# Kernel optimization log

Hardware: AMD Instinct MI355X
Metric: run time of the kernel (lower is better)

Reference implementation:

```python
import jax, jax.numpy as jnp
import numpy as np

NUM_NODES = 100000
D = 256            # node_hidden_dim
H = 256            # edge_hidden_dim
P = 524288         # num_pairs


def setup_inputs() -> dict:
    key = jax.random.key(0)
    k1, k2, k3, k4, k5, k6 = jax.random.split(key, 6)
    h_nodes = jax.random.normal(k1, (NUM_NODES, D), dtype=jnp.float32)
    dst = jax.random.randint(k2, (P,), 0, NUM_NODES, dtype=jnp.int64)
    src = jax.random.randint(k3, (P,), 0, NUM_NODES, dtype=jnp.int64)
    # Bias-free MLP weights, stored as [in, out] so forward is x @ W
    s1 = 1.0 / np.sqrt(2 * D)
    s2 = 1.0 / np.sqrt(H)
    W1 = jax.random.uniform(k4, (2 * D, H), jnp.float32, -s1, s1)
    W2 = jax.random.uniform(k5, (H, H), jnp.float32, -s2, s2)
    W3 = jax.random.uniform(k6, (H, 2), jnp.float32, -s2, s2)
    return {"h_nodes": h_nodes, "dst": dst, "src": src, "W1": W1, "W2": W2, "W3": W3}


def reference(h_nodes, dst, src, W1, W2, W3):
    # gather src/dst embeddings and concat -> [P, 2D]
    h_pair = jnp.concatenate([h_nodes[dst], h_nodes[src]], axis=-1)
    x = jax.nn.relu(h_pair @ W1)   # [P, H]
    x = jax.nn.relu(x @ W2)        # [P, H]
    return x @ W3                  # [P, 2] edge logits
```

## Files before the change

kernel.cpp:

```cpp
#include <hip/hip_runtime.h>
#include <stdint.h>

typedef __attribute__((ext_vector_type(8))) short short8;
typedef __attribute__((ext_vector_type(4))) short short4v;
typedef __attribute__((ext_vector_type(4))) float floatx4;

__device__ __forceinline__ unsigned short f2bf(float x) {
  unsigned int u = __float_as_uint(x);
  u += 0x7fffu + ((u >> 16) & 1u);
  return (unsigned short)(u >> 16);
}
__device__ __forceinline__ float bf2f(unsigned short b) {
  return __uint_as_float(((unsigned int)b) << 16);
}
__device__ __forceinline__ int sw3(int r) { return (r & 7) ^ (((r >> 3) & 1) * 3); }

__global__ void prep_kernel(const float* __restrict__ h, const float* __restrict__ W1,
                            const float* __restrict__ W2, const float* __restrict__ W3,
                            unsigned short* __restrict__ HBF, unsigned short* __restrict__ W1F,
                            unsigned short* __restrict__ W2F, unsigned short* __restrict__ W3F,
                            int nh4) {
  const int t = threadIdx.x;
  int b = blockIdx.x;
  if (b < 512) {
    int u = b * 256 + t;
    int j = u & 7, kq = (u >> 3) & 3, n = (u >> 5) & 255, k32 = u >> 13;
    W1F[u] = f2bf(W1[(k32 * 32 + kq * 8 + j) * 256 + n]);
    return;
  }
  b -= 512;
  if (b < 256) {
    int u = b * 256 + t;
    int j = u & 7, kq = (u >> 3) & 3, n = (u >> 5) & 255, k32 = u >> 13;
    W2F[u] = f2bf(W2[(k32 * 32 + kq * 8 + j) * 256 + n]);
    return;
  }
  b -= 256;
  if (b < 16) {
    int u = b * 256 + t;
    int j = u & 7, L = (u >> 3) & 63, k32 = u >> 9;
    int n = L & 15, kq = L >> 4;
    W3F[u] = (n < 2) ? f2bf(W3[(k32 * 32 + kq * 8 + j) * 2 + n]) : (unsigned short)0;
    return;
  }
  b -= 16;
  int u = b * 256 + t;
  if (u < nh4) {
    float4 v = ((const float4*)h)[u];
    short4v s;
    s[0] = (short)f2bf(v.x); s[1] = (short)f2bf(v.y);
    s[2] = (short)f2bf(v.z); s[3] = (short)f2bf(v.w);
    ((short4v*)HBF)[u] = s;
  }
}

__global__ __launch_bounds__(256, 2)
void edge_mlp3(const unsigned short* __restrict__ hbf,
               const int* __restrict__ dst,
               const int* __restrict__ src,
               const unsigned short* __restrict__ W1F,
               const unsigned short* __restrict__ W2F,
               const unsigned short* __restrict__ W3F,
               float* __restrict__ out) {
  __shared__ unsigned short A[64 * 512];
  __shared__ int ioff[128];
  unsigned short* X  = A;
  unsigned short* X2 = A + 16384;

  const int t = threadIdx.x, lane = t & 63, w = t >> 6;
  const int lq = lane >> 4, lm = lane & 15;
  const int m0 = blockIdx.x * 64;

  if (t < 64)       ioff[t] = dst[m0 + t];
  else if (t < 128) ioff[t] = src[m0 + t - 64];
  __syncthreads();

  {
    const int c = lane, half = (c >= 32) ? 64 : 0, cc = c & 31;
    short8 g[16];
#pragma unroll
    for (int it = 0; it < 16; ++it) {
      int node = ioff[half + it * 4 + w];
      g[it] = ((const short8*)hbf)[node * 32 + cc];
    }
#pragma unroll
    for (int it = 0; it < 16; ++it) {
      int r = it * 4 + w;
      *(short8*)&A[r * 512 + ((c ^ sw3(r)) << 3)] = g[it];
    }
  }

  floatx4 acc[4][4];
#pragma unroll
  for (int i = 0; i < 4; ++i)
#pragma unroll
    for (int j = 0; j < 4; ++j) acc[i][j] = (floatx4)(0.0f);
  __syncthreads();

  const short8* B1 = (const short8*)W1F;
  const short8* B2 = (const short8*)W2F;

  {
    short8 bq[4][4];
#pragma unroll
    for (int s = 0; s < 4; ++s)
#pragma unroll
      for (int jt = 0; jt < 4; ++jt)
        bq[s][jt] = B1[(s * 256 + w * 64 + jt * 16 + lm) * 4 + lq];

#pragma unroll
    for (int s = 0; s < 16; ++s) {
#pragma unroll
      for (int i = 0; i < 4; ++i) {
        int r = i * 16 + lm, cch = s * 4 + lq;
        short8 af = *(const short8*)&A[r * 512 + ((cch ^ sw3(r)) << 3)];
#pragma unroll
        for (int j = 0; j < 4; ++j)
          acc[i][j] = __builtin_amdgcn_mfma_f32_16x16x32_bf16(af, bq[s & 3][j], acc[i][j], 0, 0, 0);
      }
      if (s < 12)
#pragma unroll
        for (int jt = 0; jt < 4; ++jt)
          bq[s & 3][jt] = B1[((s + 4) * 256 + w * 64 + jt * 16 + lm) * 4 + lq];
    }
  }
  __syncthreads();
#pragma unroll
  for (int i = 0; i < 4; ++i) {
    int row0 = i * 16 + lq * 4;
#pragma unroll
    for (int j = 0; j < 4; ++j) {
      int col = w * 64 + j * 16 + lm, c8 = col >> 3, ce = col & 7;
#pragma unroll
      for (int rg = 0; rg < 4; ++rg) {
        int row = row0 + rg;
        float v = acc[i][j][rg];
        v = v > 0.0f ? v : 0.0f;
        X[row * 256 + (((c8 ^ sw3(row)) << 3) | ce)] = f2bf(v);
      }
    }
  }
#pragma unroll
  for (int i = 0; i < 4; ++i)
#pragma unroll
    for (int j = 0; j < 4; ++j) acc[i][j] = (floatx4)(0.0f);
  __syncthreads();

  {
    short8 bq[4][4];
#pragma unroll
    for (int s = 0; s < 4; ++s)
#pragma unroll
      for (int jt = 0; jt < 4; ++jt)
        bq[s][jt] = B2[(s * 256 + w * 64 + jt * 16 + lm) * 4 + lq];

#pragma unroll
    for (int s = 0; s < 8; ++s) {
#pragma unroll
      for (int i = 0; i < 4; ++i) {
        int r = i * 16 + lm, cch = s * 4 + lq;
        short8 af = *(const short8*)&X[r * 256 + ((cch ^ sw3(r)) << 3)];
#pragma unroll
        for (int j = 0; j < 4; ++j)
          acc[i][j] = __builtin_amdgcn_mfma_f32_16x16x32_bf16(af, bq[s & 3][j], acc[i][j], 0, 0, 0);
      }
      if (s < 4)
#pragma unroll
        for (int jt = 0; jt < 4; ++jt)
          bq[s & 3][jt] = B2[((s + 4) * 256 + w * 64 + jt * 16 + lm) * 4 + lq];
    }
  }
  __syncthreads();
#pragma unroll
  for (int i = 0; i < 4; ++i) {
    int row0 = i * 16 + lq * 4;
#pragma unroll
    for (int j = 0; j < 4; ++j) {
      int col = w * 64 + j * 16 + lm, c8 = col >> 3, ce = col & 7;
#pragma unroll
      for (int rg = 0; rg < 4; ++rg) {
        int row = row0 + rg;
        float v = acc[i][j][rg];
        v = v > 0.0f ? v : 0.0f;
        X2[row * 256 + (((c8 ^ sw3(row)) << 3) | ce)] = f2bf(v);
      }
    }
  }
  __syncthreads();

  {
    floatx4 a3 = (floatx4)(0.0f);
    const short8* B3 = (const short8*)W3F;
#pragma unroll
    for (int s = 0; s < 8; ++s) {
      short8 b3 = B3[s * 64 + lane];
      int r = w * 16 + lm, cch = s * 4 + lq;
      short8 af = *(const short8*)&X2[r * 256 + ((cch ^ sw3(r)) << 3)];
      a3 = __builtin_amdgcn_mfma_f32_16x16x32_bf16(af, b3, a3, 0, 0, 0);
    }
    if (lm < 2) {
#pragma unroll
      for (int rg = 0; rg < 4; ++rg)
        out[(m0 + w * 16 + lq * 4 + rg) * 2 + lm] = a3[rg];
    }
  }
}

__global__ void wfrag_kernel(const float* __restrict__ W,
                             unsigned short* __restrict__ out, int total) {
  int u = blockIdx.x * 256 + threadIdx.x;
  if (u >= total) return;
  int j = u & 7, kq = (u >> 3) & 3, n = (u >> 5) & 255, k32 = u >> 13;
  out[u] = f2bf(W[(k32 * 32 + kq * 8 + j) * 256 + n]);
}

__global__ __launch_bounds__(256, 2)
void edge_mlp_fb(const float* __restrict__ h,
                 const int* __restrict__ dst,
                 const int* __restrict__ src,
                 const unsigned short* __restrict__ W1F,
                 const unsigned short* __restrict__ W2F,
                 const float* __restrict__ W3,
                 float* __restrict__ out) {
  __shared__ unsigned short A[64 * 512];
  __shared__ float w3s[512];
  __shared__ int ioff[128];
  unsigned short* X = A;
  const int t = threadIdx.x, lane = t & 63, w = t >> 6;
  const int lq = lane >> 4, lm = lane & 15;
  const int m0 = blockIdx.x * 64;
  if (t < 64) ioff[t] = dst[m0 + t];
  else if (t < 128) ioff[t] = src[m0 + t - 64];
  w3s[t] = W3[t];
  w3s[t + 256] = W3[t + 256];
  __syncthreads();
  {
    const int c = lane, half = (c >= 32) ? 64 : 0, cc = c & 31;
#pragma unroll
    for (int it = 0; it < 16; ++it) {
      int r = it * 4 + w;
      int node = ioff[half + r];
      const float4* h4 = (const float4*)h;
      float4 v0 = h4[node * 64 + cc * 2], v1 = h4[node * 64 + cc * 2 + 1];
      short8 v;
      v[0] = (short)f2bf(v0.x); v[1] = (short)f2bf(v0.y);
      v[2] = (short)f2bf(v0.z); v[3] = (short)f2bf(v0.w);
      v[4] = (short)f2bf(v1.x); v[5] = (short)f2bf(v1.y);
      v[6] = (short)f2bf(v1.z); v[7] = (short)f2bf(v1.w);
      *(short8*)&A[r * 512 + ((c ^ (r & 7)) << 3)] = v;
    }
  }
  floatx4 acc[4][4];
#pragma unroll
  for (int i = 0; i < 4; ++i)
#pragma unroll
    for (int j = 0; j < 4; ++j) acc[i][j] = (floatx4)(0.0f);
  __syncthreads();
  const short8* B1 = (const short8*)W1F;
  const short8* B2 = (const short8*)W2F;
#pragma unroll
  for (int k32 = 0; k32 < 16; ++k32) {
    short8 b[4], af[4];
#pragma unroll
    for (int jt = 0; jt < 4; ++jt)
      b[jt] = B1[(k32 * 256 + w * 64 + jt * 16 + lm) * 4 + lq];
#pragma unroll
    for (int i = 0; i < 4; ++i) {
      int r = i * 16 + lm, c = k32 * 4 + lq;
      af[i] = *(const short8*)&A[r * 512 + ((c ^ (r & 7)) << 3)];
    }
#pragma unroll
    for (int i = 0; i < 4; ++i)
#pragma unroll
      for (int j = 0; j < 4; ++j)
        acc[i][j] = __builtin_amdgcn_mfma_f32_16x16x32_bf16(af[i], b[j], acc[i][j], 0, 0, 0);
  }
  __syncthreads();
#pragma unroll
  for (int i = 0; i < 4; ++i) {
    int row0 = i * 16 + lq * 4;
#pragma unroll
    for (int j = 0; j < 4; ++j) {
      int col = w * 64 + j * 16 + lm, c8 = col >> 3, ce = col & 7;
#pragma unroll
      for (int rg = 0; rg < 4; ++rg) {
        int row = row0 + rg;
        float v = acc[i][j][rg];
        v = v > 0.0f ? v : 0.0f;
        X[row * 256 + (((c8 ^ (row & 7)) << 3) | ce)] = f2bf(v);
      }
    }
  }
#pragma unroll
  for (int i = 0; i < 4; ++i)
#pragma unroll
    for (int j = 0; j < 4; ++j) acc[i][j] = (floatx4)(0.0f);
  __syncthreads();
#pragma unroll
  for (int k32 = 0; k32 < 8; ++k32) {
    short8 b[4], af[4];
#pragma unroll
    for (int jt = 0; jt < 4; ++jt)
      b[jt] = B2[(k32 * 256 + w * 64 + jt * 16 + lm) * 4 + lq];
#pragma unroll
    for (int i = 0; i < 4; ++i) {
      int r = i * 16 + lm, c = k32 * 4 + lq;
      af[i] = *(const short8*)&X[r * 256 + ((c ^ (r & 7)) << 3)];
    }
#pragma unroll
    for (int i = 0; i < 4; ++i)
#pragma unroll
      for (int j = 0; j < 4; ++j)
        acc[i][j] = __builtin_amdgcn_mfma_f32_16x16x32_bf16(af[i], b[j], acc[i][j], 0, 0, 0);
  }
  __syncthreads();
#pragma unroll
  for (int i = 0; i < 4; ++i) {
    int row0 = i * 16 + lq * 4;
#pragma unroll
    for (int j = 0; j < 4; ++j) {
      int col = w * 64 + j * 16 + lm, c8 = col >> 3, ce = col & 7;
#pragma unroll
      for (int rg = 0; rg < 4; ++rg) {
        int row = row0 + rg;
        float v = acc[i][j][rg];
        v = v > 0.0f ? v : 0.0f;
        X[row * 256 + (((c8 ^ (row & 7)) << 3) | ce)] = f2bf(v);
      }
    }
  }
  __syncthreads();
  {
    int r = t >> 2, o = (t >> 1) & 1, hh = t & 1;
    float s = 0.0f;
#pragma unroll
    for (int it = 0; it < 16; ++it) {
      int c = hh * 16 + it;
      short8 xv = *(const short8*)&X[r * 256 + ((c ^ (r & 7)) << 3)];
#pragma unroll
      for (int e = 0; e < 8; ++e)
        s += bf2f((unsigned short)xv[e]) * w3s[((c << 3) + e) * 2 + o];
    }
    s += __shfl_xor(s, 1);
    if (hh == 0) out[(m0 + r) * 2 + o] = s;
  }
}

extern "C" void kernel_launch(void* const* d_in, const int* in_sizes, int n_in,
                              void* d_out, int out_size, void* d_ws, size_t ws_size,
                              hipStream_t stream) {
  const float* h   = (const float*)d_in[0];
  const int*   dst = (const int*)d_in[1];
  const int*   src = (const int*)d_in[2];
  const float* W1  = (const float*)d_in[3];
  const float* W2  = (const float*)d_in[4];
  const float* W3  = (const float*)d_in[5];
  float* out = (float*)d_out;

  const int h_elems = in_sizes[0];
  const int n_pairs = in_sizes[1];
  const int ntiles  = n_pairs / 64;

  const size_t hbf_elems = (size_t)h_elems;
  const bool use_hbf =
      ws_size >= (hbf_elems + 131072 + 65536 + 4096) * sizeof(unsigned short);

  unsigned short* HBF = (unsigned short*)d_ws;
  unsigned short* W1F = HBF + hbf_elems;
  unsigned short* W2F = W1F + 131072;
  unsigned short* W3F = W2F + 65536;

  if (use_hbf) {
    int nh4 = h_elems / 4;
    int grid = 512 + 256 + 16 + (nh4 + 255) / 256;
    prep_kernel<<<grid, 256, 0, stream>>>(h, W1, W2, W3, HBF, W1F, W2F, W3F, nh4);
    edge_mlp3<<<ntiles, 256, 0, stream>>>(HBF, dst, src, W1F, W2F, W3F, out);
  } else {
    unsigned short* W1Fb = (unsigned short*)d_ws;
    unsigned short* W2Fb = W1Fb + 131072;
    wfrag_kernel<<<512, 256, 0, stream>>>(W1, W1Fb, 131072);
    wfrag_kernel<<<256, 256, 0, stream>>>(W2, W2Fb, 65536);
    edge_mlp_fb<<<ntiles, 256, 0, stream>>>(h, dst, src, W1Fb, W2Fb, W3, out);
  }
}
```

Baseline: 410.1 us.

## Make edge MLP persistent with register-resident weights and async LDS gather prefetch

Replaces the one-tile-per-block kernel with a persistent 512-thread kernel over a 256-block grid. Each wave holds its slice of W1 and W2 in registers for the whole run, so weights are no longer reloaded from global memory for every tile. The node-embedding gather for the next tile is issued with global_load_lds into a double-buffered, padded LDS tile while the current tile runs its matmuls, and indices are prefetched two tiles ahead. The cost is heavy register pressure from the resident weights, which may cause spills or lower occupancy, plus more LDS per block and only 256 blocks to cover all CUs.

```diff
diff --git a/kernel.cpp b/kernel.cpp
--- a/kernel.cpp
+++ b/kernel.cpp
@@ -14,6 +14,11 @@
   return __uint_as_float(((unsigned int)b) << 16);
 }
 __device__ __forceinline__ int sw3(int r) { return (r & 7) ^ (((r >> 3) & 1) * 3); }
+__device__ __forceinline__ void gload_lds16(const void* g, void* lds) {
+  __builtin_amdgcn_global_load_lds(
+      (const __attribute__((address_space(1))) unsigned int*)g,
+      (__attribute__((address_space(3))) unsigned int*)lds, 16, 0, 0);
+}
 
 __global__ void prep_kernel(const float* __restrict__ h, const float* __restrict__ W1,
                             const float* __restrict__ W2, const float* __restrict__ W3,
@@ -54,154 +59,163 @@
   }
 }
 
-__global__ __launch_bounds__(256, 2)
-void edge_mlp3(const unsigned short* __restrict__ hbf,
+__global__ __launch_bounds__(512, 2)
+void edge_mlp4(const unsigned short* __restrict__ hbf,
                const int* __restrict__ dst,
                const int* __restrict__ src,
                const unsigned short* __restrict__ W1F,
                const unsigned short* __restrict__ W2F,
                const unsigned short* __restrict__ W3F,
-               float* __restrict__ out) {
-  __shared__ unsigned short A[64 * 512];
-  __shared__ int ioff[128];
-  unsigned short* X  = A;
-  unsigned short* X2 = A + 16384;
+               float* __restrict__ out, int ntiles) {
+  __shared__ unsigned char AB[2][66560];
+  __shared__ int iobuf[2][128];
 
   const int t = threadIdx.x, lane = t & 63, w = t >> 6;
   const int lq = lane >> 4, lm = lane & 15;
-  const int m0 = blockIdx.x * 64;
-
-  if (t < 64)       ioff[t] = dst[m0 + t];
-  else if (t < 128) ioff[t] = src[m0 + t - 64];
-  __syncthreads();
-
-  {
-    const int c = lane, half = (c >= 32) ? 64 : 0, cc = c & 31;
-    short8 g[16];
-#pragma unroll
-    for (int it = 0; it < 16; ++it) {
-      int node = ioff[half + it * 4 + w];
-      g[it] = ((const short8*)hbf)[node * 32 + cc];
-    }
-#pragma unroll
-    for (int it = 0; it < 16; ++it) {
-      int r = it * 4 + w;
-      *(short8*)&A[r * 512 + ((c ^ sw3(r)) << 3)] = g[it];
-    }
-  }
-
-  floatx4 acc[4][4];
-#pragma unroll
-  for (int i = 0; i < 4; ++i)
-#pragma unroll
-    for (int j = 0; j < 4; ++j) acc[i][j] = (floatx4)(0.0f);
-  __syncthreads();
+  const int bid = blockIdx.x, stride = gridDim.x;
+  const int nIter = (ntiles - bid + stride - 1) / stride;
+  const int last = nIter - 1;
 
   const short8* B1 = (const short8*)W1F;
   const short8* B2 = (const short8*)W2F;
+  short8 w1r[16][2], w2r[8][2];
+#pragma unroll
+  for (int s = 0; s < 16; ++s)
+#pragma unroll
+    for (int j = 0; j < 2; ++j)
+      w1r[s][j] = B1[(s * 256 + w * 32 + j * 16 + lm) * 4 + lq];
+#pragma unroll
+  for (int s = 0; s < 8; ++s)
+#pragma unroll
+    for (int j = 0; j < 2; ++j)
+      w2r[s][j] = B2[(s * 256 + w * 32 + j * 16 + lm) * 4 + lq];
+
+  if (t < 128) {
+    const int* p = (t < 64) ? dst : src;
+    int i0 = t & 63;
+    iobuf[0][t] = p[bid * 64 + i0];
+    if (last >= 1) iobuf[1][t] = p[(bid + stride) * 64 + i0];
+  }
+  __syncthreads();
 
   {
-    short8 bq[4][4];
-#pragma unroll
-    for (int s = 0; s < 4; ++s)
-#pragma unroll
-      for (int jt = 0; jt < 4; ++jt)
-        bq[s][jt] = B1[(s * 256 + w * 64 + jt * 16 + lm) * 4 + lq];
+    const int li = lane & 31;
+#pragma unroll
+    for (int u = 0; u < 8; ++u) {
+      int r = w * 8 + u;
+      int node = (lane < 32) ? iobuf[0][r] : iobuf[0][64 + r];
+      gload_lds16((const char*)hbf + (size_t)node * 512 + li * 16, &AB[0][r * 1040]);
+    }
+  }
+
+  for (int T = 0; T < nIter; ++T) {
+    const int cur = T & 1, nxt = cur ^ 1;
+    const int m0 = (bid + T * stride) * 64;
+    __syncthreads();
+
+    if (T < last) {
+      const int li = lane & 31;
+#pragma unroll
+      for (int u = 0; u < 8; ++u) {
+        int r = w * 8 + u;
+        int node = (lane < 32) ? iobuf[nxt][r] : iobuf[nxt][64 + r];
+        gload_lds16((const char*)hbf + (size_t)node * 512 + li * 16, &AB[nxt][r * 1040]);
+      }
+    }
+
+    floatx4 acc[4][2];
+#pragma unroll
+    for (int i = 0; i < 4; ++i)
+#pragma unroll
+      for (int j = 0; j < 2; ++j) acc[i][j] = (floatx4)(0.0f);
 
 #pragma unroll
     for (int s = 0; s < 16; ++s) {
 #pragma unroll
       for (int i = 0; i < 4; ++i) {
-        int r = i * 16 + lm, cch = s * 4 + lq;
-        short8 af = *(const short8*)&A[r * 512 + ((cch ^ sw3(r)) << 3)];
-#pragma unroll
-        for (int j = 0; j < 4; ++j)
-          acc[i][j] = __builtin_amdgcn_mfma_f32_16x16x32_bf16(af, bq[s & 3][j], acc[i][j], 0, 0, 0);
-      }
-      if (s < 12)
-#pragma unroll
-        for (int jt = 0; jt < 4; ++jt)
-          bq[s & 3][jt] = B1[((s + 4) * 256 + w * 64 + jt * 16 + lm) * 4 + lq];
-    }
-  }
-  __syncthreads();
-#pragma unroll
-  for (int i = 0; i < 4; ++i) {
-    int row0 = i * 16 + lq * 4;
-#pragma unroll
-    for (int j = 0; j < 4; ++j) {
-      int col = w * 64 + j * 16 + lm, c8 = col >> 3, ce = col & 7;
-#pragma unroll
-      for (int rg = 0; rg < 4; ++rg) {
-        int row = row0 + rg;
-        float v = acc[i][j][rg];
-        v = v > 0.0f ? v : 0.0f;
-        X[row * 256 + (((c8 ^ sw3(row)) << 3) | ce)] = f2bf(v);
-      }
-    }
-  }
-#pragma unroll
-  for (int i = 0; i < 4; ++i)
-#pragma unroll
-    for (int j = 0; j < 4; ++j) acc[i][j] = (floatx4)(0.0f);
-  __syncthreads();
-
-  {
-    short8 bq[4][4];
-#pragma unroll
-    for (int s = 0; s < 4; ++s)
-#pragma unroll
-      for (int jt = 0; jt < 4; ++jt)
-        bq[s][jt] = B2[(s * 256 + w * 64 + jt * 16 + lm) * 4 + lq];
+        int r = i * 16 + lm;
+        short8 af = *(const short8*)&AB[cur][r * 1040 + (s * 4 + lq) * 16];
+        acc[i][0] = __builtin_amdgcn_mfma_f32_16x16x32_bf16(af, w1r[s][0], acc[i][0], 0, 0, 0);
+        acc[i][1] = __builtin_amdgcn_mfma_f32_16x16x32_bf16(af, w1r[s][1], acc[i][1], 0, 0, 0);
+      }
+    }
+
+    int idxv = 0;
+    const bool doidx = (T + 2 <= last) && (t < 128);
+    if (doidx) {
+      const int* p = (t < 64) ? dst : src;
+      idxv = p[(bid + (T + 2) * stride) * 64 + (t & 63)];
+    }
+
+    __syncthreads();
+
+    unsigned short* X = (unsigned short*)&AB[cur][0];
+#pragma unroll
+    for (int i = 0; i < 4; ++i) {
+      int row0 = i * 16 + lq * 4;
+#pragma unroll
+      for (int j = 0; j < 2; ++j) {
+        int col = w * 32 + j * 16 + lm, c8 = col >> 3, ce = col & 7;
+#pragma unroll
+        for (int rg = 0; rg < 4; ++rg) {
+          int row = row0 + rg;
+          float v = acc[i][j][rg];
+          v = v > 0.0f ? v : 0.0f;
+          X[row * 256 + (((c8 ^ sw3(row)) << 3) | ce)] = f2bf(v);
+        }
+      }
+    }
+    if (doidx) iobuf[cur][t] = idxv;
+#pragma unroll
+    for (int i = 0; i < 4; ++i)
+#pragma unroll
+      for (int j = 0; j < 2; ++j) acc[i][j] = (floatx4)(0.0f);
+    __syncthreads();
 
 #pragma unroll
     for (int s = 0; s < 8; ++s) {
 #pragma unroll
       for (int i = 0; i < 4; ++i) {
-        int r = i * 16 + lm, cch = s * 4 + lq;
-        short8 af = *(const short8*)&X[r * 256 + ((cch ^ sw3(r)) << 3)];
-#pragma unroll
-        for (int j = 0; j < 4; ++j)
-          acc[i][j] = __builtin_amdgcn_mfma_f32_16x16x32_bf16(af, bq[s & 3][j], acc[i][j], 0, 0, 0);
-      }
-      if (s < 4)
-#pragma unroll
-        for (int jt = 0; jt < 4; ++jt)
-          bq[s & 3][jt] = B2[((s + 4) * 256 + w * 64 + jt * 16 + lm) * 4 + lq];
-    }
-  }
-  __syncthreads();
-#pragma unroll
-  for (int i = 0; i < 4; ++i) {
-    int row0 = i * 16 + lq * 4;
-#pragma unroll
-    for (int j = 0; j < 4; ++j) {
-      int col = w * 64 + j * 16 + lm, c8 = col >> 3, ce = col & 7;
-#pragma unroll
-      for (int rg = 0; rg < 4; ++rg) {
-        int row = row0 + rg;
-        float v = acc[i][j][rg];
-        v = v > 0.0f ? v : 0.0f;
-        X2[row * 256 + (((c8 ^ sw3(row)) << 3) | ce)] = f2bf(v);
-      }
-    }
-  }
-  __syncthreads();
-
-  {
-    floatx4 a3 = (floatx4)(0.0f);
-    const short8* B3 = (const short8*)W3F;
-#pragma unroll
-    for (int s = 0; s < 8; ++s) {
-      short8 b3 = B3[s * 64 + lane];
-      int r = w * 16 + lm, cch = s * 4 + lq;
-      short8 af = *(const short8*)&X2[r * 256 + ((cch ^ sw3(r)) << 3)];
-      a3 = __builtin_amdgcn_mfma_f32_16x16x32_bf16(af, b3, a3, 0, 0, 0);
-    }
-    if (lm < 2) {
-#pragma unroll
-      for (int rg = 0; rg < 4; ++rg)
-        out[(m0 + w * 16 + lq * 4 + rg) * 2 + lm] = a3[rg];
+        int r = i * 16 + lm;
+        short8 af = *(const short8*)&X[r * 256 + (((s * 4 + lq) ^ sw3(r)) << 3)];
+        acc[i][0] = __builtin_amdgcn_mfma_f32_16x16x32_bf16(af, w2r[s][0], acc[i][0], 0, 0, 0);
+        acc[i][1] = __builtin_amdgcn_mfma_f32_16x16x32_bf16(af, w2r[s][1], acc[i][1], 0, 0, 0);
+      }
+    }
+    __syncthreads();
+
+#pragma unroll
+    for (int i = 0; i < 4; ++i) {
+      int row0 = i * 16 + lq * 4;
+#pragma unroll
+      for (int j = 0; j < 2; ++j) {
+        int col = w * 32 + j * 16 + lm, c8 = col >> 3, ce = col & 7;
+#pragma unroll
+        for (int rg = 0; rg < 4; ++rg) {
+          int row = row0 + rg;
+          float v = acc[i][j][rg];
+          v = v > 0.0f ? v : 0.0f;
+          X[row * 256 + (((c8 ^ sw3(row)) << 3) | ce)] = f2bf(v);
+        }
+      }
+    }
+    __syncthreads();
+
+    if (w < 4) {
+      floatx4 a3 = (floatx4)(0.0f);
+      const short8* B3 = (const short8*)W3F;
+#pragma unroll
+      for (int s = 0; s < 8; ++s) {
+        short8 b3 = B3[s * 64 + lane];
+        int r = w * 16 + lm;
+        short8 af = *(const short8*)&X[r * 256 + (((s * 4 + lq) ^ sw3(r)) << 3)];
+        a3 = __builtin_amdgcn_mfma_f32_16x16x32_bf16(af, b3, a3, 0, 0, 0);
+      }
+      if (lm < 2) {
+#pragma unroll
+        for (int rg = 0; rg < 4; ++rg)
+          out[(m0 + w * 16 + lq * 4 + rg) * 2 + lm] = a3[rg];
+      }
     }
   }
 }
@@ -374,7 +388,8 @@
     int nh4 = h_elems / 4;
     int grid = 512 + 256 + 16 + (nh4 + 255) / 256;
     prep_kernel<<<grid, 256, 0, stream>>>(h, W1, W2, W3, HBF, W1F, W2F, W3F, nh4);
-    edge_mlp3<<<ntiles, 256, 0, stream>>>(HBF, dst, src, W1F, W2F, W3F, out);
+    int pgrid = ntiles < 256 ? ntiles : 256;
+    edge_mlp4<<<pgrid, 512, 0, stream>>>(HBF, dst, src, W1F, W2F, W3F, out, ntiles);
   } else {
     unsigned short* W1Fb = (unsigned short*)d_ws;
     unsigned short* W2Fb = W1Fb + 131072;
```

Measured after the change: 789.9 us. 1.93x slower.
